# Kernel optimization log

Hardware: AMD Instinct MI355X
Metric: run time of the kernel (lower is better)

The kernel has to match this reference:

```python
import math
import jax, jax.numpy as jnp
import numpy as np

TAU = 0.5  # RelaxedOneHotCategorical temperature


def setup_inputs() -> dict:
    key = jax.random.key(0)
    k1, k2, k3 = jax.random.split(key, 3)
    B, T, D, K = 64, 2048, 128, 512
    inputs = jax.random.normal(k1, (B, T, D), dtype=jnp.float32)
    # uniform noise driving the gumbel-softmax rsample (one per (token, code))
    u = jax.random.uniform(k2, (B * T, K), dtype=jnp.float32)
    # codebook init: uniform(-1/K, 1/K) as in the torch module
    embedding = jax.random.uniform(k3, (K, D), dtype=jnp.float32,
                                   minval=-1.0 / K, maxval=1.0 / K)
    return {"inputs": inputs, "u": u, "embedding": embedding}


def reference(inputs, u, embedding):
    K, D = embedding.shape
    flat = inputs.reshape(-1, D)  # [N, D]

    # squared-euclidean distances: [N, K]
    distances = ((flat ** 2).sum(axis=1, keepdims=True)
                 + (embedding ** 2).sum(axis=1)
                 - 2.0 * flat @ embedding.T)
    logits = -distances

    # normalized log-probs / probs of the categorical (dist.logits / dist.probs)
    logp = jax.nn.log_softmax(logits, axis=1)
    probs = jnp.exp(logp)

    # RelaxedOneHotCategorical(0.5).rsample(): softmax((logits + gumbel)/tau)
    tiny = jnp.finfo(u.dtype).tiny
    gumbel = -jnp.log(-jnp.log(jnp.clip(u, tiny, 1.0 - 1e-7)))
    encodings = jax.nn.softmax((logits + gumbel) / TAU, axis=1)  # [N, K]

    # weighted codebook lookup + straight-through estimator
    quantized = (encodings @ embedding).reshape(inputs.shape)
    quantized = inputs + jax.lax.stop_gradient(quantized - inputs)

    # KL(q || uniform) with zero-prob masking; sum over tokens, mean over codes
    kl = probs * (logp + math.log(K))
    kl = jnp.where(probs == 0, 0.0, kl)
    KL = kl.sum(axis=0).mean()

    # perplexity of the soft code usage
    avg_probs = encodings.mean(axis=0)
    perplexity = jnp.exp(-jnp.sum(avg_probs * jnp.log(avg_probs + 1e-10)))

    return (KL, quantized, perplexity, encodings)
```

## Files before the change

### kernel.cpp

```cpp
#include <hip/hip_runtime.h>
#include <stdint.h>

#define N_TOK 131072
#define KC    512
#define DIM   128
#define LOGK  6.2383246250395075f
#define CLIP_HI 0.99999988079071044921875f
#define CLIP_LO 1.17549435e-38f
#define NLN2x2  -1.3862943611198906f

typedef float  f32x4 __attribute__((ext_vector_type(4)));
typedef short  s16x8 __attribute__((ext_vector_type(8)));

__device__ __forceinline__ unsigned short f2bf(float f) {
  unsigned int b = __float_as_uint(f);
  b = b + 0x7FFFu + ((b >> 16) & 1u);
  return (unsigned short)(b >> 16);
}

__device__ __forceinline__ float prec_ln(float u) {
  int i = __float_as_int(u);
  int k = (i - 0x3F3504F3) >> 23;
  float m = __int_as_float(i - (k << 23));
  float s  = (m - 1.0f) * __builtin_amdgcn_rcpf(m + 1.0f);
  float s2 = s * s;
  float p  = fmaf(fmaf(fmaf(0.22222222f, s2, 0.28571429f), s2, 0.4f), s2, 0.66666667f);
  return fmaf((float)k, 0.69314718f, fmaf(s * s2, p, 2.0f * s));
}

__global__ void prep_kernel(const float* __restrict__ emb,
                            unsigned short* __restrict__ EF,
                            unsigned short* __restrict__ ETF,
                            float* __restrict__ normE) {
  int k = blockIdx.x;
  int d = threadIdx.x;
  int j = ((k & 31) << 4) | (k >> 5);
  float v = emb[k * DIM + d];
  unsigned short h = f2bf(v);
  {
    int w  = j >> 8, nt = (j >> 4) & 15, c0 = j & 15;
    int db = d >> 5, q = (d >> 3) & 3, e = d & 7;
    EF[((((size_t)(w * 16 + nt) * 4 + db) * 64) + (q * 16 + c0)) * 8 + e] = h;
  }
  {
    int w2 = d >> 6, n2 = (d >> 4) & 3, c0 = d & 15;
    int kb = j >> 5, q = (j >> 3) & 3, e = j & 7;
    ETF[((((size_t)(w2 * 4 + n2) * 16 + kb) * 64) + (q * 16 + c0)) * 8 + e] = h;
  }
  __shared__ float red[128];
  red[d] = v * v;
  __syncthreads();
  for (int s = 64; s > 0; s >>= 1) { if (d < s) red[d] += red[d + s]; __syncthreads(); }
  if (d == 0) normE[j] = red[0];
}

__global__ __launch_bounds__(128, 4) void vq_main(
    const float* __restrict__ X, const float* __restrict__ U,
    const unsigned short* __restrict__ EF, const unsigned short* __restrict__ ETF,
    const float* __restrict__ normE,
    float* __restrict__ out_q, float* __restrict__ out_enc,
    float* __restrict__ avgp_rep, float* __restrict__ kl_rep)
{
  const int tid  = threadIdx.x;
  const int w    = tid >> 6;
  const int lane = tid & 63;
  const int q    = lane >> 4;
  const int c0   = lane & 15;
  const int wg   = blockIdx.x;
  const int rowbase = wg * 16;

  __shared__ float xs[5][2][16];
  __shared__ unsigned short encT[16][520];

  s16x8 afrag[4];
  {
    const float* xrow = X + (size_t)(rowbase + c0) * DIM;
    #pragma unroll
    for (int db = 0; db < 4; db++) {
      const float4 v0 = *reinterpret_cast<const float4*>(xrow + db * 32 + q * 8);
      const float4 v1 = *reinterpret_cast<const float4*>(xrow + db * 32 + q * 8 + 4);
      s16x8 u8;
      u8[0] = (short)f2bf(v0.x); u8[1] = (short)f2bf(v0.y);
      u8[2] = (short)f2bf(v0.z); u8[3] = (short)f2bf(v0.w);
      u8[4] = (short)f2bf(v1.x); u8[5] = (short)f2bf(v1.y);
      u8[6] = (short)f2bf(v1.z); u8[7] = (short)f2bf(v1.w);
      afrag[db] = u8;
    }
  }

  f32x4 acc[16];
  const unsigned short* efw = EF + (size_t)w * (16 * 4 * 64 * 8);
  #pragma unroll
  for (int nt = 0; nt < 16; nt++) {
    f32x4 a = {0.f, 0.f, 0.f, 0.f};
    #pragma unroll
    for (int db = 0; db < 4; db++) {
      s16x8 b = *reinterpret_cast<const s16x8*>(efw + ((size_t)(nt * 4 + db) * 64 + lane) * 8);
      a = __builtin_amdgcn_mfma_f32_16x16x32_bf16(afrag[db], b, a, 0, 0, 0);
    }
    acc[nt] = a;
  }
  #pragma unroll
  for (int nt = 0; nt < 16; nt++) {
    float ne = normE[(w * 16 + nt) * 16 + c0];
    acc[nt] = acc[nt] * 2.f - ne;
  }

  #pragma unroll
  for (int r = 0; r < 4; r++) {
    const int rr = q * 4 + r;
    float m = acc[0][r];
    #pragma unroll
    for (int nt = 1; nt < 16; nt++) m = fmaxf(m, acc[nt][r]);
    #pragma unroll
    for (int mm = 1; mm <= 8; mm <<= 1) m = fmaxf(m, __shfl_xor(m, mm));
    float Z = 0.f, W = 0.f;
    #pragma unroll
    for (int nt = 0; nt < 16; nt++) {
      float dd = acc[nt][r] - m;
      float e  = __expf(dd);
      Z += e; W = fmaf(e, dd, W);
    }
    #pragma unroll
    for (int mm = 1; mm <= 8; mm <<= 1) { Z += __shfl_xor(Z, mm); W += __shfl_xor(W, mm); }
    if (c0 == 0) { xs[0][w][rr] = m; xs[1][w][rr] = Z; xs[2][w][rr] = W; }

    const float* urow = U + (size_t)(rowbase + rr) * KC + c0 * 32 + w * 16;
    float m2 = -3.4e38f;
    #pragma unroll
    for (int tt = 0; tt < 4; tt++) {
      float4 u4 = *reinterpret_cast<const float4*>(urow + 4 * tt);
      #pragma unroll
      for (int jj = 0; jj < 4; jj++) {
        float uv = (&u4.x)[jj];
        uv = fminf(fmaxf(uv, CLIP_LO), CLIP_HI);
        float t  = -prec_ln(uv);
        float g2 = NLN2x2 * __log2f(t);
        float y  = fmaf(2.0f, acc[4 * tt + jj][r], g2);
        acc[4 * tt + jj][r] = y;
        m2 = fmaxf(m2, y);
      }
    }
    #pragma unroll
    for (int mm = 1; mm <= 8; mm <<= 1) m2 = fmaxf(m2, __shfl_xor(m2, mm));
    float Z2 = 0.f;
    #pragma unroll
    for (int nt = 0; nt < 16; nt++) {
      float p = __expf(acc[nt][r] - m2);
      acc[nt][r] = p;
      Z2 += p;
    }
    #pragma unroll
    for (int mm = 1; mm <= 8; mm <<= 1) Z2 += __shfl_xor(Z2, mm);
    if (c0 == 0) { xs[3][w][rr] = m2; xs[4][w][rr] = Z2; }
  }
  __syncthreads();

  if (tid < 16) {
    float m0 = xs[0][0][tid], m1 = xs[0][1][tid];
    float mg = fmaxf(m0, m1);
    float s0 = __expf(m0 - mg), s1 = __expf(m1 - mg);
    float Z  = fmaf(s0, xs[1][0][tid], s1 * xs[1][1][tid]);
    float Wv = s0 * fmaf(m0 - mg, xs[1][0][tid], xs[2][0][tid])
             + s1 * fmaf(m1 - mg, xs[1][1][tid], xs[2][1][tid]);
    float kl = Wv / Z - prec_ln(Z) + LOGK;
    #pragma unroll
    for (int mm = 1; mm <= 8; mm <<= 1) kl += __shfl_xor(kl, mm);
    if (tid == 0) atomicAdd(&kl_rep[wg & 31], kl);
  }

  float rzv[4];
  #pragma unroll
  for (int r = 0; r < 4; r++) {
    const int rr = q * 4 + r;
    float m20 = xs[3][0][rr], m21 = xs[3][1][rr];
    float m2g = fmaxf(m20, m21);
    float Z2g = fmaf(__expf(m20 - m2g), xs[4][0][rr], __expf(m21 - m2g) * xs[4][1][rr]);
    float mw  = w ? m21 : m20;
    rzv[r] = __expf(mw - m2g) * __builtin_amdgcn_rcpf(Z2g);
  }

  {
    float avg_acc[16];
    #pragma unroll
    for (int nt = 0; nt < 16; nt++) avg_acc[nt] = 0.f;

    #pragma unroll
    for (int r = 0; r < 4; r++) {
      float* erow = out_enc + (size_t)(rowbase + q * 4 + r) * KC + c0 * 32 + w * 16;
      #pragma unroll
      for (int tt = 0; tt < 4; tt++) {
        float4 ev;
        #pragma unroll
        for (int jj = 0; jj < 4; jj++) {
          float enc = acc[4 * tt + jj][r] * rzv[r];
          (&ev.x)[jj] = enc;
          avg_acc[4 * tt + jj] += enc;
        }
        *reinterpret_cast<float4*>(erow + 4 * tt) = ev;
        #pragma unroll
        for (int jj = 0; jj < 4; jj++) {
          float enc = (&ev.x)[jj];
          float pv = __shfl_xor(enc, 1);
          if (!(lane & 1)) {
            unsigned int pk = (unsigned int)f2bf(enc) | ((unsigned int)f2bf(pv) << 16);
            *reinterpret_cast<unsigned int*>(
                &encT[q * 4 + r][(w * 16 + 4 * tt + jj) * 16 + c0]) = pk;
          }
        }
      }
    }

    #pragma unroll
    for (int nt = 0; nt < 16; nt++) {
      float v = avg_acc[nt];
      v += __shfl_xor(v, 16);
      v += __shfl_xor(v, 32);
      if (lane < 16)
        atomicAdd(&avgp_rep[(size_t)(wg & 31) * KC + (w * 16 + nt) * 16 + lane], v);
    }
  }
  __syncthreads();

  f32x4 accq[4];
  #pragma unroll
  for (int n2 = 0; n2 < 4; n2++) accq[n2] = {0.f, 0.f, 0.f, 0.f};
  #pragma unroll
  for (int kb = 0; kb < 16; kb++) {
    s16x8 af = *reinterpret_cast<const s16x8*>(&encT[c0][kb * 32 + q * 8]);
    #pragma unroll
    for (int n2 = 0; n2 < 4; n2++) {
      s16x8 b = *reinterpret_cast<const s16x8*>(
          ETF + ((size_t)((w * 4 + n2) * 16 + kb) * 64 + lane) * 8);
      accq[n2] = __builtin_amdgcn_mfma_f32_16x16x32_bf16(af, b, accq[n2], 0, 0, 0);
    }
  }
  #pragma unroll
  for (int n2 = 0; n2 < 4; n2++) {
    #pragma unroll
    for (int r = 0; r < 4; r++) {
      int grow = rowbase + q * 4 + r;
      out_q[(size_t)grow * DIM + w * 64 + n2 * 16 + c0] = accq[n2][r];
    }
  }
}

__global__ void finalize_kernel(const float* __restrict__ avgp_rep,
                                const float* __restrict__ kl_rep,
                                float* __restrict__ d_out) {
  __shared__ float red[512];
  int t = threadIdx.x;
  float s = 0.f;
  for (int rsl = 0; rsl < 32; rsl++) s += avgp_rep[rsl * KC + t];
  float avg = s * (1.0f / (float)N_TOK);
  red[t] = avg * logf(avg + 1e-10f);
  __syncthreads();
  for (int st = 256; st > 0; st >>= 1) { if (t < st) red[t] += red[t + st]; __syncthreads(); }
  if (t == 0) {
    d_out[1 + (size_t)N_TOK * DIM] = __expf(-red[0]);
    float kl = 0.f;
    for (int i2 = 0; i2 < 32; i2++) kl += kl_rep[i2];
    d_out[0] = kl * (1.0f / (float)KC);
  }
}

extern "C" void kernel_launch(void* const* d_in, const int* in_sizes, int n_in,
                              void* d_out, int out_size, void* d_ws, size_t ws_size,
                              hipStream_t stream) {
  const float* X = (const float*)d_in[0];
  const float* U = (const float*)d_in[1];
  const float* E = (const float*)d_in[2];
  float* out = (float*)d_out;

  char* ws = (char*)d_ws;
  unsigned short* EF     = (unsigned short*)(ws);
  unsigned short* ETF    = (unsigned short*)(ws + 131072);
  float*          normE  = (float*)(ws + 262144);
  float*          avgp_r = (float*)(ws + 264192);
  float*          kl_r   = (float*)(ws + 329728);

  hipMemsetAsync(ws + 264192, 0, 65536 + 128, stream);
  prep_kernel<<<512, 128, 0, stream>>>(E, EF, ETF, normE);
  vq_main<<<N_TOK / 16, 128, 0, stream>>>(X, U, EF, ETF, normE,
                                          out + 1,
                                          out + 1 + (size_t)N_TOK * DIM + 1,
                                          avgp_r, kl_r);
  finalize_kernel<<<1, 512, 0, stream>>>(avgp_r, kl_r, out);
}
```

Baseline: 694.0 us.

## Remap code-to-lane permutation for coalesced U/enc access and prefetch noise

Changes the permutation from codebook index to MFMA column so that each lane's 16 codes form four float4 groups strided by 64. Neighbouring lanes then read U and write the encodings over contiguous 64-byte spans instead of 128-byte-strided chunks. All U values are loaded into registers right after the GEMM, before the softmax, so their latency overlaps other work. normE is laid out for float4 loads. Holding U in registers raises register pressure, so launch bounds drop from 4 to 3 blocks per SIMD, which may reduce occupancy.

New measurement: 629.7 us. 1.1x faster.

```diff
diff --git a/kernel.cpp b/kernel.cpp
--- a/kernel.cpp
+++ b/kernel.cpp
@@ -31,10 +31,11 @@
 __global__ void prep_kernel(const float* __restrict__ emb,
                             unsigned short* __restrict__ EF,
                             unsigned short* __restrict__ ETF,
-                            float* __restrict__ normE) {
+                            float* __restrict__ normE2) {
   int k = blockIdx.x;
   int d = threadIdx.x;
-  int j = ((k & 31) << 4) | (k >> 5);
+  int wk = (k >> 8) & 1, tk = (k >> 6) & 3, ck = (k >> 2) & 15, jk = k & 3;
+  int j = ((wk * 16 + tk * 4 + jk) << 4) | ck;
   float v = emb[k * DIM + d];
   unsigned short h = f2bf(v);
   {
@@ -51,13 +52,13 @@
   red[d] = v * v;
   __syncthreads();
   for (int s = 64; s > 0; s >>= 1) { if (d < s) red[d] += red[d + s]; __syncthreads(); }
-  if (d == 0) normE[j] = red[0];
-}
-
-__global__ __launch_bounds__(128, 4) void vq_main(
+  if (d == 0) normE2[(j >> 8) * 256 + (j & 15) * 16 + ((j >> 4) & 15)] = red[0];
+}
+
+__global__ __launch_bounds__(128, 3) void vq_main(
     const float* __restrict__ X, const float* __restrict__ U,
     const unsigned short* __restrict__ EF, const unsigned short* __restrict__ ETF,
-    const float* __restrict__ normE,
+    const float* __restrict__ normE2,
     float* __restrict__ out_q, float* __restrict__ out_enc,
     float* __restrict__ avgp_rep, float* __restrict__ kl_rep)
 {
@@ -100,10 +101,27 @@
     }
     acc[nt] = a;
   }
-  #pragma unroll
-  for (int nt = 0; nt < 16; nt++) {
-    float ne = normE[(w * 16 + nt) * 16 + c0];
-    acc[nt] = acc[nt] * 2.f - ne;
+
+  float4 ureg[4][4];
+  {
+    const float* ub = U + (size_t)rowbase * KC + (size_t)(w * 4) * 64 + c0 * 4;
+    #pragma unroll
+    for (int r = 0; r < 4; r++)
+      #pragma unroll
+      for (int tt = 0; tt < 4; tt++)
+        ureg[r][tt] = *reinterpret_cast<const float4*>(ub + (size_t)(q * 4 + r) * KC + tt * 64);
+  }
+
+  {
+    const float* nb = normE2 + w * 256 + c0 * 16;
+    float4 nv[4];
+    #pragma unroll
+    for (int i = 0; i < 4; i++) nv[i] = *reinterpret_cast<const float4*>(nb + 4 * i);
+    #pragma unroll
+    for (int nt = 0; nt < 16; nt++) {
+      float ne = (&nv[nt >> 2].x)[nt & 3];
+      acc[nt] = acc[nt] * 2.f - ne;
+    }
   }
 
   #pragma unroll
@@ -125,14 +143,12 @@
     for (int mm = 1; mm <= 8; mm <<= 1) { Z += __shfl_xor(Z, mm); W += __shfl_xor(W, mm); }
     if (c0 == 0) { xs[0][w][rr] = m; xs[1][w][rr] = Z; xs[2][w][rr] = W; }
 
-    const float* urow = U + (size_t)(rowbase + rr) * KC + c0 * 32 + w * 16;
     float m2 = -3.4e38f;
     #pragma unroll
     for (int tt = 0; tt < 4; tt++) {
-      float4 u4 = *reinterpret_cast<const float4*>(urow + 4 * tt);
       #pragma unroll
       for (int jj = 0; jj < 4; jj++) {
-        float uv = (&u4.x)[jj];
+        float uv = (&ureg[r][tt].x)[jj];
         uv = fminf(fmaxf(uv, CLIP_LO), CLIP_HI);
         float t  = -prec_ln(uv);
         float g2 = NLN2x2 * __log2f(t);
@@ -187,7 +203,7 @@
 
     #pragma unroll
     for (int r = 0; r < 4; r++) {
-      float* erow = out_enc + (size_t)(rowbase + q * 4 + r) * KC + c0 * 32 + w * 16;
+      float* erow = out_enc + (size_t)(rowbase + q * 4 + r) * KC + (size_t)(w * 4) * 64 + c0 * 4;
       #pragma unroll
       for (int tt = 0; tt < 4; tt++) {
         float4 ev;
@@ -197,7 +213,7 @@
           (&ev.x)[jj] = enc;
           avg_acc[4 * tt + jj] += enc;
         }
-        *reinterpret_cast<float4*>(erow + 4 * tt) = ev;
+        *reinterpret_cast<float4*>(erow + tt * 64) = ev;
         #pragma unroll
         for (int jj = 0; jj < 4; jj++) {
           float enc = (&ev.x)[jj];
@@ -275,13 +291,13 @@
   char* ws = (char*)d_ws;
   unsigned short* EF     = (unsigned short*)(ws);
   unsigned short* ETF    = (unsigned short*)(ws + 131072);
-  float*          normE  = (float*)(ws + 262144);
+  float*          normE2 = (float*)(ws + 262144);
   float*          avgp_r = (float*)(ws + 264192);
   float*          kl_r   = (float*)(ws + 329728);
 
   hipMemsetAsync(ws + 264192, 0, 65536 + 128, stream);
-  prep_kernel<<<512, 128, 0, stream>>>(E, EF, ETF, normE);
-  vq_main<<<N_TOK / 16, 128, 0, stream>>>(X, U, EF, ETF, normE,
+  prep_kernel<<<512, 128, 0, stream>>>(E, EF, ETF, normE2);
+  vq_main<<<N_TOK / 16, 128, 0, stream>>>(X, U, EF, ETF, normE2,
                                           out + 1,
                                           out + 1 + (size_t)N_TOK * DIM + 1,
                                           avgp_r, kl_r);
```
